# Kernel tuning notes

Measured on AMD Instinct MI355X. Metric: run time of the kernel, lower is better.

## Reference

```python
import jax, jax.numpy as jnp
import numpy as np

EPS = 1e-5

def _bn(z, g, b):
    # train-mode BatchNorm2d: batch stats over (B,H,W), biased variance
    mean = z.mean(axis=(0, 2, 3), keepdims=True)
    var = z.var(axis=(0, 2, 3), keepdims=True)
    return g[None, :, None, None] * (z - mean) * jax.lax.rsqrt(var + EPS) + b[None, :, None, None]

def _conv1x1(x, w):
    # x: [B,C,H,W], w: [O,C] -> [B,O,H,W]
    return jnp.einsum('bchw,oc->bohw', x, w)

def _proj(x, w1, g1, b1, w2, g2, b2):
    z = _bn(_conv1x1(x, w1), g1, b1)
    return _bn(_conv1x1(z, w2), g2, b2)

def setup_inputs() -> dict:
    key = jax.random.key(0)
    ks = jax.random.split(key, 24)
    B, Cx, Cy, M, H, W = 4, 512, 256, 64, 64, 64
    f32 = jnp.float32
    def wmat(k, o, c):
        return jax.random.normal(k, (o, c), f32) * (c ** -0.5)
    def gamma(k, c):
        return 1.0 + 0.1 * jax.random.normal(k, (c,), f32)
    def beta(k, c):
        return 0.1 * jax.random.normal(k, (c,), f32)
    inp = {
        'x': jax.random.normal(ks[0], (B, Cx, H, W), f32),
        'y': jax.random.normal(ks[1], (B, Cy, H, W), f32),
        # f_self
        'ws1': wmat(ks[2], M, Cx), 'gs1': gamma(ks[3], M), 'bs1': beta(ks[4], M),
        'ws2': wmat(ks[5], M, M),  'gs2': gamma(ks[6], M), 'bs2': beta(ks[7], M),
        # f_x
        'wx1': wmat(ks[8], M, Cx), 'gx1': gamma(ks[9], M), 'bx1': beta(ks[10], M),
        'wx2': wmat(ks[11], M, M), 'gx2': gamma(ks[12], M), 'bx2': beta(ks[13], M),
        # f_y
        'wy1': wmat(ks[14], M, Cy), 'gy1': gamma(ks[15], M), 'by1': beta(ks[16], M),
        'wy2': wmat(ks[17], M, M),  'gy2': gamma(ks[18], M), 'by2': beta(ks[19], M),
        # f_up
        'wu': wmat(ks[20], Cx, M), 'gu': gamma(ks[21], Cx), 'bu': beta(ks[22], Cx),
    }
    return inp

def reference(x, y, ws1, gs1, bs1, ws2, gs2, bs2,
              wx1, gx1, bx1, wx2, gx2, bx2,
              wy1, gy1, by1, wy2, gy2, by2,
              wu, gu, bu):
    B, C, H, W = x.shape
    M = ws1.shape[0]
    N = H * W
    fself = _proj(x, ws1, gs1, bs1, ws2, gs2, bs2).reshape(B, M, N).transpose(0, 2, 1)  # [B,N,M]
    fx = _proj(x, wx1, gx1, bx1, wx2, gx2, bx2).reshape(B, M, N).transpose(0, 2, 1)      # [B,N,M]
    fy = _proj(y, wy1, gy1, by1, wy2, gy2, by2).reshape(B, M, N)                          # [B,M,N]
    sim = jnp.matmul(fx, fy)                  # [B,N,N]  (scale=False)
    attn = jax.nn.softmax(sim, axis=-1)
    fout = jnp.matmul(attn, fself)            # [B,N,M]
    fout = fout.transpose(0, 2, 1).reshape(B, M, H, W)
    out = _bn(_conv1x1(fout, wu), gu, bu)
    return x + out
```

## Files before the change

kernel.cpp:

```cpp
#include <hip/hip_runtime.h>
#include <hip/hip_fp16.h>
#include <cstdint>

constexpr int N_ = 4096;
constexpr float CNT = 16384.f;

typedef __attribute__((ext_vector_type(8))) _Float16 half8;
typedef __attribute__((ext_vector_type(4))) float f32x4;
union fragh { half8 h8; int i4[4]; };

__device__ inline int pkh(float a, float b) {
  union { __half2 h; int i; } u;
  u.h = __float22half2_rn(float2{a, b});
  return u.i;
}


__global__ __launch_bounds__(256) void conv1_k(
    const float* __restrict__ x, const float* __restrict__ y,
    const float* __restrict__ ws1, const float* __restrict__ wx1,
    const float* __restrict__ wy1,
    float* __restrict__ z1s, float* __restrict__ z1x, float* __restrict__ z1y,
    float* __restrict__ stats) {
  const int t = threadIdx.x;
  const int slice = blockIdx.x;
  const int b = slice >> 5;
  const int n0 = (slice & 31) * 128;
  const int branch = blockIdx.y;
  const float* A = branch == 2 ? y : x;
  const float* W = branch == 0 ? ws1 : (branch == 1 ? wx1 : wy1);
  float* out = branch == 0 ? z1s : (branch == 1 ? z1x : z1y);
  const int K = branch == 2 ? 256 : 512;
  float* st = stats + branch * 128;

  __shared__ float sA[32][132];
  __shared__ float sW[32][72];

  const int to = (t >> 5) * 8;
  const int tn = (t & 31) * 4;
  float acc[8][4];
#pragma unroll
  for (int i = 0; i < 8; ++i)
#pragma unroll
    for (int j = 0; j < 4; ++j) acc[i][j] = 0.f;

  const float* Ab = A + (size_t)b * K * N_ + n0;
#pragma unroll 1
  for (int k0 = 0; k0 < K; k0 += 32) {
    __syncthreads();
#pragma unroll
    for (int i = 0; i < 4; ++i) {
      int row = i * 8 + (t >> 5);
      float4 v = *(const float4*)&Ab[(size_t)(k0 + row) * N_ + tn];
      *(float4*)&sA[row][tn] = v;
    }
    {
      int o = t >> 2, kk = (t & 3) * 8;
      float4 w0 = *(const float4*)&W[(size_t)o * K + k0 + kk];
      float4 w1 = *(const float4*)&W[(size_t)o * K + k0 + kk + 4];
      sW[kk + 0][o] = w0.x; sW[kk + 1][o] = w0.y;
      sW[kk + 2][o] = w0.z; sW[kk + 3][o] = w0.w;
      sW[kk + 4][o] = w1.x; sW[kk + 5][o] = w1.y;
      sW[kk + 6][o] = w1.z; sW[kk + 7][o] = w1.w;
    }
    __syncthreads();
#pragma unroll
    for (int k = 0; k < 32; ++k) {
      float4 a = *(const float4*)&sA[k][tn];
      float4 w0 = *(const float4*)&sW[k][to];
      float4 w1 = *(const float4*)&sW[k][to + 4];
      float wv[8] = {w0.x, w0.y, w0.z, w0.w, w1.x, w1.y, w1.z, w1.w};
      float av[4] = {a.x, a.y, a.z, a.w};
#pragma unroll
      for (int i = 0; i < 8; ++i)
#pragma unroll
        for (int j = 0; j < 4; ++j) acc[i][j] += wv[i] * av[j];
    }
  }
  float* Cb = out + (size_t)b * 64 * N_ + n0;
#pragma unroll
  for (int i = 0; i < 8; ++i) {
    float4 v = {acc[i][0], acc[i][1], acc[i][2], acc[i][3]};
    *(float4*)&Cb[(size_t)(to + i) * N_ + tn] = v;
  }
#pragma unroll
  for (int i = 0; i < 8; ++i) {
    float s = acc[i][0] + acc[i][1] + acc[i][2] + acc[i][3];
    float q = acc[i][0] * acc[i][0] + acc[i][1] * acc[i][1] +
              acc[i][2] * acc[i][2] + acc[i][3] * acc[i][3];
#pragma unroll
    for (int d = 1; d < 32; d <<= 1) { s += __shfl_xor(s, d); q += __shfl_xor(q, d); }
    if ((t & 31) == 0) { atomicAdd(&st[to + i], s); atomicAdd(&st[64 + to + i], q); }
  }
}

__global__ __launch_bounds__(256) void conv2_k(
    const float* __restrict__ z1s, const float* __restrict__ z1x,
    const float* __restrict__ z1y,
    const float* __restrict__ ws2, const float* __restrict__ wx2,
    const float* __restrict__ wy2,
    const float* __restrict__ gs1, const float* __restrict__ bs1,
    const float* __restrict__ gx1, const float* __restrict__ bx1,
    const float* __restrict__ gy1, const float* __restrict__ by1,
    float* __restrict__ z2s, float* __restrict__ z2x, float* __restrict__ z2y,
    float* __restrict__ stats) {
  const int t = threadIdx.x;
  const int slice = blockIdx.x;
  const int b = slice >> 5;
  const int n0 = (slice & 31) * 128;
  const int branch = blockIdx.y;
  const float* A = branch == 0 ? z1s : (branch == 1 ? z1x : z1y);
  const float* W = branch == 0 ? ws2 : (branch == 1 ? wx2 : wy2);
  const float* g1 = branch == 0 ? gs1 : (branch == 1 ? gx1 : gy1);
  const float* b1 = branch == 0 ? bs1 : (branch == 1 ? bx1 : by1);
  float* out = branch == 0 ? z2s : (branch == 1 ? z2x : z2y);
  const float* stin = stats + branch * 128;
  float* stout = stats + (3 + branch) * 128;

  __shared__ float sA[32][132];
  __shared__ float sW[32][72];
  __shared__ float sc[64], sh[64];

  if (t < 64) {
    float mean = stin[t] * (1.f / CNT);
    float var = stin[64 + t] * (1.f / CNT) - mean * mean;
    float r = rsqrtf(var + 1e-5f);
    float s = g1[t] * r;
    sc[t] = s;
    sh[t] = b1[t] - mean * s;
  }

  const int to = (t >> 5) * 8;
  const int tn = (t & 31) * 4;
  float acc[8][4];
#pragma unroll
  for (int i = 0; i < 8; ++i)
#pragma unroll
    for (int j = 0; j < 4; ++j) acc[i][j] = 0.f;

  const float* Ab = A + (size_t)b * 64 * N_ + n0;
#pragma unroll 1
  for (int k0 = 0; k0 < 64; k0 += 32) {
    __syncthreads();
#pragma unroll
    for (int i = 0; i < 4; ++i) {
      int row = i * 8 + (t >> 5);
      float4 v = *(const float4*)&Ab[(size_t)(k0 + row) * N_ + tn];
      float s = sc[k0 + row], h = sh[k0 + row];
      v.x = v.x * s + h; v.y = v.y * s + h; v.z = v.z * s + h; v.w = v.w * s + h;
      *(float4*)&sA[row][tn] = v;
    }
    {
      int o = t >> 2, kk = (t & 3) * 8;
      float4 w0 = *(const float4*)&W[(size_t)o * 64 + k0 + kk];
      float4 w1 = *(const float4*)&W[(size_t)o * 64 + k0 + kk + 4];
      sW[kk + 0][o] = w0.x; sW[kk + 1][o] = w0.y;
      sW[kk + 2][o] = w0.z; sW[kk + 3][o] = w0.w;
      sW[kk + 4][o] = w1.x; sW[kk + 5][o] = w1.y;
      sW[kk + 6][o] = w1.z; sW[kk + 7][o] = w1.w;
    }
    __syncthreads();
#pragma unroll
    for (int k = 0; k < 32; ++k) {
      float4 a = *(const float4*)&sA[k][tn];
      float4 w0 = *(const float4*)&sW[k][to];
      float4 w1 = *(const float4*)&sW[k][to + 4];
      float wv[8] = {w0.x, w0.y, w0.z, w0.w, w1.x, w1.y, w1.z, w1.w};
      float av[4] = {a.x, a.y, a.z, a.w};
#pragma unroll
      for (int i = 0; i < 8; ++i)
#pragma unroll
        for (int j = 0; j < 4; ++j) acc[i][j] += wv[i] * av[j];
    }
  }
  float* Cb = out + (size_t)b * 64 * N_ + n0;
#pragma unroll
  for (int i = 0; i < 8; ++i) {
    float4 v = {acc[i][0], acc[i][1], acc[i][2], acc[i][3]};
    *(float4*)&Cb[(size_t)(to + i) * N_ + tn] = v;
  }
#pragma unroll
  for (int i = 0; i < 8; ++i) {
    float s = acc[i][0] + acc[i][1] + acc[i][2] + acc[i][3];
    float q = acc[i][0] * acc[i][0] + acc[i][1] * acc[i][1] +
              acc[i][2] * acc[i][2] + acc[i][3] * acc[i][3];
#pragma unroll
    for (int d = 1; d < 32; d <<= 1) { s += __shfl_xor(s, d); q += __shfl_xor(q, d); }
    if ((t & 31) == 0) { atomicAdd(&stout[to + i], s); atomicAdd(&stout[64 + to + i], q); }
  }
}

__global__ __launch_bounds__(256) void pack_k(
    const float* __restrict__ z2s, const float* __restrict__ z2x,
    const float* __restrict__ z2y,
    const float* __restrict__ gs2, const float* __restrict__ bs2,
    const float* __restrict__ gx2, const float* __restrict__ bx2,
    const float* __restrict__ gy2, const float* __restrict__ by2,
    int* __restrict__ Qh, int* __restrict__ Kh, int* __restrict__ Vp,
    const float* __restrict__ stats) {
  const int job = blockIdx.z;
  const int idx = blockIdx.x * 256 + threadIdx.x;
  const float* z2 = job == 0 ? z2x : (job == 1 ? z2y : z2s);
  const float* g2 = job == 0 ? gx2 : (job == 1 ? gy2 : gs2);
  const float* b2 = job == 0 ? bx2 : (job == 1 ? by2 : bs2);
  const float* st = stats + (job == 0 ? 4 : (job == 1 ? 5 : 3)) * 128;
  int* outp = job == 0 ? Qh : (job == 1 ? Kh : Vp);

  auto snorm = [&](int c, float& s, float& h) {
    float mean = st[c] * (1.f / CNT);
    float var = st[64 + c] * (1.f / CNT) - mean * mean;
    float r = rsqrtf(var + 1e-5f);
    s = g2[c] * r;
    h = b2[c] - mean * s;
  };
  if (job < 2) {
    int n = idx & 4095, c = (idx >> 12) & 31, b = idx >> 17;
    float s0, h0, s1, h1;
    snorm(2 * c, s0, h0);
    snorm(2 * c + 1, s1, h1);
    float v0 = z2[((size_t)b * 64 + 2 * c) * N_ + n] * s0 + h0;
    float v1 = z2[((size_t)b * 64 + 2 * c + 1) * N_ + n] * s1 + h1;
    outp[idx] = pkh(v0, v1);
  } else {
    int k = idx & 2047, ch = (idx >> 11) & 63, b = idx >> 17;
    float s0, h0;
    snorm(ch, s0, h0);
    float2 v = *(const float2*)&z2[((size_t)b * 64 + ch) * N_ + 2 * k];
    outp[idx] = pkh(v.x * s0 + h0, v.y * s0 + h0);
  }
}

__global__ __launch_bounds__(256) void attn_k(const int* __restrict__ Qh,
                                              const int* __restrict__ Kh,
                                              const int* __restrict__ Vp,
                                              float* __restrict__ fout) {
  const int tid = threadIdx.x;
  const int lane = tid & 63;
  const int wid = tid >> 6;
  const int la = lane & 15;
  const int quad = lane >> 4;
  const int b = blockIdx.x & 3;
  const int qbase = (blockIdx.x >> 2) * 16;
  const int* Qb = Qh + (size_t)b * 32 * N_;
  const int* Kb = Kh + (size_t)b * 32 * N_;
  const int* Vb = Vp + (size_t)b * 64 * 2048;

  __shared__ union USm {
    float P[4][16 * 36];
    struct { float O[4][16][68]; float M[4][16]; float L[4][16]; } e;
  } smu;
  float* myP = smu.P[wid];

  fragh aq[2];
#pragma unroll
  for (int c = 0; c < 2; ++c)
#pragma unroll
    for (int j = 0; j < 4; ++j)
      aq[c].i4[j] = Qb[(size_t)(c * 16 + quad * 4 + j) * N_ + qbase + la];

  f32x4 o[4];
  float mrun[4], lrun[4];
#pragma unroll
  for (int mt = 0; mt < 4; ++mt) o[mt] = f32x4{0.f, 0.f, 0.f, 0.f};
#pragma unroll
  for (int r = 0; r < 4; ++r) { mrun[r] = -3.0e38f; lrun[r] = 0.f; }

  const int jbeg = wid * (N_ / 4);
#pragma unroll 1
  for (int j0 = jbeg; j0 < jbeg + N_ / 4; j0 += 32) {
    f32x4 s[2];
#pragma unroll
    for (int nt = 0; nt < 2; ++nt) {
      fragh k0, k1;
      const int key = j0 + nt * 16 + la;
#pragma unroll
      for (int jj = 0; jj < 4; ++jj) {
        k0.i4[jj] = Kb[(size_t)(quad * 4 + jj) * N_ + key];
        k1.i4[jj] = Kb[(size_t)(16 + quad * 4 + jj) * N_ + key];
      }
      f32x4 z = f32x4{0.f, 0.f, 0.f, 0.f};
      z = __builtin_amdgcn_mfma_f32_16x16x32_f16(aq[0].h8, k0.h8, z, 0, 0, 0);
      s[nt] = __builtin_amdgcn_mfma_f32_16x16x32_f16(aq[1].h8, k1.h8, z, 0, 0, 0);
    }
    float alpha[4];
#pragma unroll
    for (int r = 0; r < 4; ++r) {
      float t = fmaxf(s[0][r], s[1][r]);
      t = fmaxf(t, __shfl_xor(t, 1));
      t = fmaxf(t, __shfl_xor(t, 2));
      t = fmaxf(t, __shfl_xor(t, 4));
      t = fmaxf(t, __shfl_xor(t, 8));
      float mnew = fmaxf(mrun[r], t);
      alpha[r] = __expf(mrun[r] - mnew);
      float p0 = __expf(s[0][r] - mnew);
      float p1 = __expf(s[1][r] - mnew);
      s[0][r] = p0; s[1][r] = p1;
      float ps = p0 + p1;
      ps += __shfl_xor(ps, 1);
      ps += __shfl_xor(ps, 2);
      ps += __shfl_xor(ps, 4);
      ps += __shfl_xor(ps, 8);
      lrun[r] = lrun[r] * alpha[r] + ps;
      mrun[r] = mnew;
    }
#pragma unroll
    for (int nt = 0; nt < 2; ++nt)
#pragma unroll
      for (int r = 0; r < 4; ++r)
        myP[(quad * 4 + r) * 36 + nt * 16 + la] = s[nt][r];
    __asm__ __volatile__("s_waitcnt lgkmcnt(0)" ::: "memory");
    fragh pa;
    {
      const f32x4* pr = (const f32x4*)&myP[la * 36 + quad * 8];
      f32x4 p0 = pr[0], p1 = pr[1];
      pa.i4[0] = pkh(p0[0], p0[1]);
      pa.i4[1] = pkh(p0[2], p0[3]);
      pa.i4[2] = pkh(p1[0], p1[1]);
      pa.i4[3] = pkh(p1[2], p1[3]);
    }
#pragma unroll
    for (int mt = 0; mt < 4; ++mt)
#pragma unroll
      for (int r = 0; r < 4; ++r) o[mt][r] *= alpha[r];
#pragma unroll
    for (int mt = 0; mt < 4; ++mt) {
      const int4 vv = *(const int4*)&Vb[(size_t)(mt * 16 + la) * 2048 + (j0 >> 1) + quad * 4];
      fragh vb;
      vb.i4[0] = vv.x; vb.i4[1] = vv.y; vb.i4[2] = vv.z; vb.i4[3] = vv.w;
      o[mt] = __builtin_amdgcn_mfma_f32_16x16x32_f16(pa.h8, vb.h8, o[mt], 0, 0, 0);
    }
  }

  __syncthreads();
  if (la == 0) {
#pragma unroll
    for (int r = 0; r < 4; ++r) {
      smu.e.M[wid][quad * 4 + r] = mrun[r];
      smu.e.L[wid][quad * 4 + r] = lrun[r];
    }
  }
#pragma unroll
  for (int mt = 0; mt < 4; ++mt)
#pragma unroll
    for (int r = 0; r < 4; ++r) smu.e.O[wid][quad * 4 + r][mt * 16 + la] = o[mt][r];
  __syncthreads();

#pragma unroll
  for (int t = 0; t < 4; ++t) {
    int oidx = t * 256 + tid;
    int m = oidx >> 4;
    int q = oidx & 15;
    float m0 = fmaxf(fmaxf(smu.e.M[0][q], smu.e.M[1][q]),
                     fmaxf(smu.e.M[2][q], smu.e.M[3][q]));
    float num = 0.f, den = 0.f;
#pragma unroll
    for (int w = 0; w < 4; ++w) {
      float wgt = __expf(smu.e.M[w][q] - m0);
      num += wgt * smu.e.O[w][q][m];
      den += wgt * smu.e.L[w][q];
    }
    fout[((size_t)b * 64 + m) * N_ + qbase + q] = num / den;
  }
}

__global__ __launch_bounds__(256) void convup_k(const float* __restrict__ fout,
                                                const float* __restrict__ wu,
                                                float* __restrict__ u,
                                                float* __restrict__ stats) {
  const int t = threadIdx.x;
  const int slice = blockIdx.x;
  const int b = slice >> 5;
  const int n0 = (slice & 31) * 128;
  const int o0 = blockIdx.y * 64;

  __shared__ float sA[32][132];
  __shared__ float sW[32][72];

  const int to = (t >> 5) * 8;
  const int tn = (t & 31) * 4;
  float acc[8][4];
#pragma unroll
  for (int i = 0; i < 8; ++i)
#pragma unroll
    for (int j = 0; j < 4; ++j) acc[i][j] = 0.f;

  const float* Ab = fout + (size_t)b * 64 * N_ + n0;
#pragma unroll 1
  for (int k0 = 0; k0 < 64; k0 += 32) {
    __syncthreads();
#pragma unroll
    for (int i = 0; i < 4; ++i) {
      int row = i * 8 + (t >> 5);
      float4 v = *(const float4*)&Ab[(size_t)(k0 + row) * N_ + tn];
      *(float4*)&sA[row][tn] = v;
    }
    {
      int o = t >> 2, kk = (t & 3) * 8;
      float4 w0 = *(const float4*)&wu[(size_t)(o0 + o) * 64 + k0 + kk];
      float4 w1 = *(const float4*)&wu[(size_t)(o0 + o) * 64 + k0 + kk + 4];
      sW[kk + 0][o] = w0.x; sW[kk + 1][o] = w0.y;
      sW[kk + 2][o] = w0.z; sW[kk + 3][o] = w0.w;
      sW[kk + 4][o] = w1.x; sW[kk + 5][o] = w1.y;
      sW[kk + 6][o] = w1.z; sW[kk + 7][o] = w1.w;
    }
    __syncthreads();
#pragma unroll
    for (int k = 0; k < 32; ++k) {
      float4 a = *(const float4*)&sA[k][tn];
      float4 w0 = *(const float4*)&sW[k][to];
      float4 w1 = *(const float4*)&sW[k][to + 4];
      float wv[8] = {w0.x, w0.y, w0.z, w0.w, w1.x, w1.y, w1.z, w1.w};
      float av[4] = {a.x, a.y, a.z, a.w};
#pragma unroll
      for (int i = 0; i < 8; ++i)
#pragma unroll
        for (int j = 0; j < 4; ++j) acc[i][j] += wv[i] * av[j];
    }
  }
  float* Cb = u + ((size_t)b * 512 + o0) * N_ + n0;
#pragma unroll
  for (int i = 0; i < 8; ++i) {
    float4 v = {acc[i][0], acc[i][1], acc[i][2], acc[i][3]};
    *(float4*)&Cb[(size_t)(to + i) * N_ + tn] = v;
  }
#pragma unroll
  for (int i = 0; i < 8; ++i) {
    float s = acc[i][0] + acc[i][1] + acc[i][2] + acc[i][3];
    float q = acc[i][0] * acc[i][0] + acc[i][1] * acc[i][1] +
              acc[i][2] * acc[i][2] + acc[i][3] * acc[i][3];
#pragma unroll
    for (int d = 1; d < 32; d <<= 1) { s += __shfl_xor(s, d); q += __shfl_xor(q, d); }
    if ((t & 31) == 0) {
      atomicAdd(&stats[768 + o0 + to + i], s);
      atomicAdd(&stats[1280 + o0 + to + i], q);
    }
  }
}

__global__ __launch_bounds__(256) void final_k(const float* __restrict__ x,
                                               const float* __restrict__ u,
                                               const float* __restrict__ gu,
                                               const float* __restrict__ bu,
                                               const float* __restrict__ stats,
                                               float* __restrict__ out) {
  size_t idx = (size_t)blockIdx.x * 256 + threadIdx.x;
  int c = (int)((idx >> 12) & 511);
  float mean = stats[768 + c] * (1.f / CNT);
  float var = stats[1280 + c] * (1.f / CNT) - mean * mean;
  float r = rsqrtf(var + 1e-5f);
  float s = gu[c] * r;
  float sh = bu[c] - mean * s;
  out[idx] = x[idx] + u[idx] * s + sh;
}

extern "C" void kernel_launch(void* const* d_in, const int* in_sizes, int n_in,
                              void* d_out, int out_size, void* d_ws, size_t ws_size,
                              hipStream_t stream) {
  const float* x = (const float*)d_in[0];
  const float* y = (const float*)d_in[1];
  const float* ws1 = (const float*)d_in[2];
  const float* gs1 = (const float*)d_in[3];
  const float* bs1 = (const float*)d_in[4];
  const float* ws2 = (const float*)d_in[5];
  const float* gs2 = (const float*)d_in[6];
  const float* bs2 = (const float*)d_in[7];
  const float* wx1 = (const float*)d_in[8];
  const float* gx1 = (const float*)d_in[9];
  const float* bx1 = (const float*)d_in[10];
  const float* wx2 = (const float*)d_in[11];
  const float* gx2 = (const float*)d_in[12];
  const float* bx2 = (const float*)d_in[13];
  const float* wy1 = (const float*)d_in[14];
  const float* gy1 = (const float*)d_in[15];
  const float* by1 = (const float*)d_in[16];
  const float* wy2 = (const float*)d_in[17];
  const float* gy2 = (const float*)d_in[18];
  const float* by2 = (const float*)d_in[19];
  const float* wu = (const float*)d_in[20];
  const float* gu = (const float*)d_in[21];
  const float* bu = (const float*)d_in[22];
  float* out = (float*)d_out;

  float* w = (float*)d_ws;
  const size_t M1 = 1048576;
  float* z1s = w + 0 * M1;
  float* z1x = w + 1 * M1;
  float* z1y = w + 2 * M1;
  float* z2s = w + 3 * M1;
  float* z2x = w + 4 * M1;
  float* z2y = w + 5 * M1;
  float* fout = w + 6 * M1;
  float* u = w + 7 * M1;
  int* Qh = (int*)(w + 15 * M1);
  int* Kh = Qh + 524288;
  int* Vp = Kh + 524288;
  float* stats = (float*)(Vp + 524288);

  hipMemsetAsync(stats, 0, 1792 * sizeof(float), stream);

  conv1_k<<<dim3(128, 3), dim3(256), 0, stream>>>(x, y, ws1, wx1, wy1, z1s, z1x,
                                                  z1y, stats);
  conv2_k<<<dim3(128, 3), dim3(256), 0, stream>>>(
      z1s, z1x, z1y, ws2, wx2, wy2, gs1, bs1, gx1, bx1, gy1, by1, z2s, z2x, z2y,
      stats);
  pack_k<<<dim3(2048, 1, 3), dim3(256), 0, stream>>>(z2s, z2x, z2y, gs2, bs2, gx2,
                                                     bx2, gy2, by2, Qh, Kh, Vp,
                                                     stats);
  attn_k<<<dim3(1024), dim3(256), 0, stream>>>(Qh, Kh, Vp, fout);
  convup_k<<<dim3(128, 8), dim3(256), 0, stream>>>(fout, wu, u, stats);
  final_k<<<dim3(32768), dim3(256), 0, stream>>>(x, u, gu, bu, stats, out);
}
```

Baseline: 426.6 us.

## Transpose attention MFMA operands so softmax rows live per lane

Swaps the MFMA operand order in the attention kernel so the score tile comes out transposed. Each lane then holds one query row, so the row max and sum need only two cross-lane shuffles instead of a 16-lane reduction for each of four rows. The P tile is packed to fp16 before it is written to LDS, which halves LDS traffic and removes the fp32 staging and repacking. The output accumulator layout changes with it, so the epilogue writes to shared memory are re-indexed.

Result: faster. 400.5 us (-6.1%).

```diff
diff --git a/kernel.cpp b/kernel.cpp
--- a/kernel.cpp
+++ b/kernel.cpp
@@ -246,10 +246,10 @@
   const int* Vb = Vp + (size_t)b * 64 * 2048;
 
   __shared__ union USm {
-    float P[4][16 * 36];
+    int P16[4][16 * 20];
     struct { float O[4][16][68]; float M[4][16]; float L[4][16]; } e;
   } smu;
-  float* myP = smu.P[wid];
+  int* myP = smu.P16[wid];
 
   fragh aq[2];
 #pragma unroll
@@ -259,11 +259,9 @@
       aq[c].i4[j] = Qb[(size_t)(c * 16 + quad * 4 + j) * N_ + qbase + la];
 
   f32x4 o[4];
-  float mrun[4], lrun[4];
+  float mrun = -3.0e38f, lrun = 0.f;
 #pragma unroll
   for (int mt = 0; mt < 4; ++mt) o[mt] = f32x4{0.f, 0.f, 0.f, 0.f};
-#pragma unroll
-  for (int r = 0; r < 4; ++r) { mrun[r] = -3.0e38f; lrun[r] = 0.f; }
 
   const int jbeg = wid * (N_ / 4);
 #pragma unroll 1
@@ -279,70 +277,61 @@
         k1.i4[jj] = Kb[(size_t)(16 + quad * 4 + jj) * N_ + key];
       }
       f32x4 z = f32x4{0.f, 0.f, 0.f, 0.f};
-      z = __builtin_amdgcn_mfma_f32_16x16x32_f16(aq[0].h8, k0.h8, z, 0, 0, 0);
-      s[nt] = __builtin_amdgcn_mfma_f32_16x16x32_f16(aq[1].h8, k1.h8, z, 0, 0, 0);
-    }
-    float alpha[4];
-#pragma unroll
-    for (int r = 0; r < 4; ++r) {
-      float t = fmaxf(s[0][r], s[1][r]);
-      t = fmaxf(t, __shfl_xor(t, 1));
-      t = fmaxf(t, __shfl_xor(t, 2));
-      t = fmaxf(t, __shfl_xor(t, 4));
-      t = fmaxf(t, __shfl_xor(t, 8));
-      float mnew = fmaxf(mrun[r], t);
-      alpha[r] = __expf(mrun[r] - mnew);
-      float p0 = __expf(s[0][r] - mnew);
-      float p1 = __expf(s[1][r] - mnew);
-      s[0][r] = p0; s[1][r] = p1;
-      float ps = p0 + p1;
-      ps += __shfl_xor(ps, 1);
-      ps += __shfl_xor(ps, 2);
-      ps += __shfl_xor(ps, 4);
-      ps += __shfl_xor(ps, 8);
-      lrun[r] = lrun[r] * alpha[r] + ps;
-      mrun[r] = mnew;
-    }
+      z = __builtin_amdgcn_mfma_f32_16x16x32_f16(k0.h8, aq[0].h8, z, 0, 0, 0);
+      s[nt] = __builtin_amdgcn_mfma_f32_16x16x32_f16(k1.h8, aq[1].h8, z, 0, 0, 0);
+    }
+    float t0 = fmaxf(fmaxf(s[0][0], s[0][1]), fmaxf(s[0][2], s[0][3]));
+    float t1 = fmaxf(fmaxf(s[1][0], s[1][1]), fmaxf(s[1][2], s[1][3]));
+    float t = fmaxf(t0, t1);
+    t = fmaxf(t, __shfl_xor(t, 16));
+    t = fmaxf(t, __shfl_xor(t, 32));
+    float mnew = fmaxf(mrun, t);
+    float alpha = __expf(mrun - mnew);
+    float p[2][4];
+    float ps = 0.f;
 #pragma unroll
     for (int nt = 0; nt < 2; ++nt)
 #pragma unroll
-      for (int r = 0; r < 4; ++r)
-        myP[(quad * 4 + r) * 36 + nt * 16 + la] = s[nt][r];
+      for (int r = 0; r < 4; ++r) {
+        p[nt][r] = __expf(s[nt][r] - mnew);
+        ps += p[nt][r];
+      }
+    ps += __shfl_xor(ps, 16);
+    ps += __shfl_xor(ps, 32);
+    lrun = lrun * alpha + ps;
+    mrun = mnew;
+#pragma unroll
+    for (int nt = 0; nt < 2; ++nt) {
+      myP[(nt * 8 + quad * 2 + 0) * 20 + la] = pkh(p[nt][0], p[nt][1]);
+      myP[(nt * 8 + quad * 2 + 1) * 20 + la] = pkh(p[nt][2], p[nt][3]);
+    }
     __asm__ __volatile__("s_waitcnt lgkmcnt(0)" ::: "memory");
-    fragh pa;
-    {
-      const f32x4* pr = (const f32x4*)&myP[la * 36 + quad * 8];
-      f32x4 p0 = pr[0], p1 = pr[1];
-      pa.i4[0] = pkh(p0[0], p0[1]);
-      pa.i4[1] = pkh(p0[2], p0[3]);
-      pa.i4[2] = pkh(p1[0], p1[1]);
-      pa.i4[3] = pkh(p1[2], p1[3]);
-    }
-#pragma unroll
-    for (int mt = 0; mt < 4; ++mt)
-#pragma unroll
-      for (int r = 0; r < 4; ++r) o[mt][r] *= alpha[r];
+    fragh pb;
+#pragma unroll
+    for (int j = 0; j < 4; ++j) pb.i4[j] = myP[(quad * 4 + j) * 20 + la];
+#pragma unroll
+    for (int mt = 0; mt < 4; ++mt) {
+      o[mt][0] *= alpha; o[mt][1] *= alpha;
+      o[mt][2] *= alpha; o[mt][3] *= alpha;
+    }
 #pragma unroll
     for (int mt = 0; mt < 4; ++mt) {
       const int4 vv = *(const int4*)&Vb[(size_t)(mt * 16 + la) * 2048 + (j0 >> 1) + quad * 4];
       fragh vb;
       vb.i4[0] = vv.x; vb.i4[1] = vv.y; vb.i4[2] = vv.z; vb.i4[3] = vv.w;
-      o[mt] = __builtin_amdgcn_mfma_f32_16x16x32_f16(pa.h8, vb.h8, o[mt], 0, 0, 0);
+      o[mt] = __builtin_amdgcn_mfma_f32_16x16x32_f16(vb.h8, pb.h8, o[mt], 0, 0, 0);
     }
   }
 
   __syncthreads();
-  if (la == 0) {
-#pragma unroll
-    for (int r = 0; r < 4; ++r) {
-      smu.e.M[wid][quad * 4 + r] = mrun[r];
-      smu.e.L[wid][quad * 4 + r] = lrun[r];
-    }
+  if (quad == 0) {
+    smu.e.M[wid][la] = mrun;
+    smu.e.L[wid][la] = lrun;
   }
 #pragma unroll
   for (int mt = 0; mt < 4; ++mt)
 #pragma unroll
-    for (int r = 0; r < 4; ++r) smu.e.O[wid][quad * 4 + r][mt * 16 + la] = o[mt][r];
+    for (int r = 0; r < 4; ++r) smu.e.O[wid][la][mt * 16 + quad * 4 + r] = o[mt][r];
   __syncthreads();
 
 #pragma unroll
```
